# Kernel optimization log

Measured on AMD Instinct MI355X. Metric: run time of the kernel, lower is better.

Reference implementation:

```python
import jax, jax.numpy as jnp
import numpy as np

B, S = 2, 1024            # 2 packed sequences, equal length (offsets = [0, 1024, 2048])
HID, H = 2560, 32
D = HID // H              # 80
ROT = int(0.4 * D)        # 32 partial rotary dims
THETA = 10000.0
MAX_POS = 2048
CACHE_SLOTS = 4096


def setup_inputs() -> dict:
    key = jax.random.key(0)
    ks = jax.random.split(key, 8)
    T = B * S
    w = lambda k: jax.random.normal(k, (HID, HID), dtype=jnp.float32) * 0.02
    return {
        "h": jax.random.normal(ks[0], (T, HID), dtype=jnp.float32),
        "k_cache": jnp.zeros((CACHE_SLOTS, HID), dtype=jnp.float32),
        "v_cache": jnp.zeros((CACHE_SLOTS, HID), dtype=jnp.float32),
        "q_w": w(ks[1]), "q_b": jnp.zeros((HID,), jnp.float32),
        "k_w": w(ks[2]), "k_b": jnp.zeros((HID,), jnp.float32),
        "v_w": w(ks[3]), "v_b": jnp.zeros((HID,), jnp.float32),
        "dense_w": w(ks[4]), "dense_b": jnp.zeros((HID,), jnp.float32),
        "positions": jnp.tile(jnp.arange(S, dtype=jnp.int32), B),
        "offsets": jnp.array([0, S, 2 * S], dtype=jnp.int32),
        "cache_indices": jnp.arange(T, dtype=jnp.int32),
    }


def _rope_tables():
    # neox-style partial rotary tables, [MAX_POS, ROT//2]
    inv_freq = 1.0 / (THETA ** (jnp.arange(0, ROT, 2, dtype=jnp.float32) / ROT))
    freqs = jnp.arange(MAX_POS, dtype=jnp.float32)[:, None] * inv_freq[None, :]
    return jnp.cos(freqs), jnp.sin(freqs)


def _apply_rope(x, cos, sin):
    # x: [T, H, D]; cos/sin: [T, ROT//2] -> rotate first ROT dims, pass rest
    c = cos[:, None, :]
    s = sin[:, None, :]
    x1, x2, rest = x[..., : ROT // 2], x[..., ROT // 2 : ROT], x[..., ROT:]
    return jnp.concatenate([x1 * c - x2 * s, x2 * c + x1 * s, rest], axis=-1)


def reference(h, k_cache, v_cache, q_w, q_b, k_w, k_b, v_w, v_b,
              dense_w, dense_b, positions, offsets, cache_indices):
    T = h.shape[0]
    q = h @ q_w + q_b
    k = h @ k_w + k_b
    v = h @ v_w + v_b

    cos_t, sin_t = _rope_tables()
    cos = cos_t[positions]
    sin = sin_t[positions]
    q = _apply_rope(q.reshape(T, H, D), cos, sin)
    k = _apply_rope(k.reshape(T, H, D), cos, sin)
    v = v.reshape(T, H, D)

    # prompt_init path: scatter freshly-rotated K/V into the flat cache
    k_cache = k_cache.at[cache_indices].set(k.reshape(T, HID))
    v_cache = v_cache.at[cache_indices].set(v.reshape(T, HID))

    # packed_attention: causal attention within each (equal-length) sequence
    q4 = q.reshape(B, S, H, D)
    k4 = k.reshape(B, S, H, D)
    v4 = v.reshape(B, S, H, D)
    scale = D ** -0.5
    scores = jnp.einsum("bqhd,bkhd->bhqk", q4, k4) * scale
    causal = jnp.tril(jnp.ones((S, S), dtype=bool))
    scores = jnp.where(causal[None, None], scores, jnp.float32(-1e9))
    p = jax.nn.softmax(scores, axis=-1)
    o = jnp.einsum("bhqk,bkhd->bqhd", p, v4).reshape(T, HID)

    return o @ dense_w + dense_b
```

## Files before the change

kernel.cpp:

```cpp
#include <hip/hip_runtime.h>
#include <hip/hip_bf16.h>

#define Bq 2
#define Sq 1024
#define Tq 2048
#define HIDq 2560
#define Hq 32
#define Dq 80
#define NQKV 7680

typedef __bf16 bf16x8 __attribute__((ext_vector_type(8)));
typedef float f32x4 __attribute__((ext_vector_type(4)));
typedef unsigned short u16x8 __attribute__((ext_vector_type(8)));
using bf16 = __hip_bfloat16;

__device__ __forceinline__ void gload_lds16(const bf16* g, bf16* l) {
  __builtin_amdgcn_global_load_lds((const __attribute__((address_space(1))) void*)g,
                                   (__attribute__((address_space(3))) void*)l,
                                   16, 0, 0);
}

__global__ __launch_bounds__(256) void cast_h_kernel(const float* __restrict__ h,
                                                     bf16* __restrict__ hb) {
  int i = (blockIdx.x * 256 + threadIdx.x) * 4;
  float4 v = *(const float4*)(h + i);
  bf16 tmp[4];
  tmp[0] = __float2bfloat16(v.x);
  tmp[1] = __float2bfloat16(v.y);
  tmp[2] = __float2bfloat16(v.z);
  tmp[3] = __float2bfloat16(v.w);
  *(ushort4*)(hb + i) = *(ushort4*)tmp;
}

__global__ __launch_bounds__(256) void bias_concat_kernel(const float* __restrict__ qb,
                                                          const float* __restrict__ kb,
                                                          const float* __restrict__ vb,
                                                          float* __restrict__ bqkv) {
  int i = blockIdx.x * 256 + threadIdx.x;
  if (i < HIDq) bqkv[i] = qb[i];
  else if (i < 2 * HIDq) bqkv[i] = kb[i - HIDq];
  else bqkv[i] = vb[i - 2 * HIDq];
}

__global__ __launch_bounds__(256) void wtrans_kernel(const float* __restrict__ qw,
                                                     const float* __restrict__ kw,
                                                     const float* __restrict__ vw,
                                                     const float* __restrict__ dw,
                                                     bf16* __restrict__ wqkvt,
                                                     bf16* __restrict__ wdt) {
  __shared__ float tile[32][33];
  const int z = blockIdx.z;
  const float* src = (z == 0) ? qw : (z == 1) ? kw : (z == 2) ? vw : dw;
  const int n0 = blockIdx.x * 32;
  const int k0 = blockIdx.y * 32;
  const int tx = threadIdx.x, ty = threadIdx.y;
#pragma unroll
  for (int r = 0; r < 4; r++)
    tile[ty + 8 * r][tx] = src[(size_t)(k0 + ty + 8 * r) * HIDq + n0 + tx];
  __syncthreads();
  bf16* dst = (z < 3) ? (wqkvt + (size_t)z * HIDq * HIDq) : wdt;
#pragma unroll
  for (int r = 0; r < 4; r++)
    dst[(size_t)(n0 + ty + 8 * r) * HIDq + k0 + tx] = __float2bfloat16(tile[tx][ty + 8 * r]);
}

__global__ __launch_bounds__(512, 2) void gemm9s_kernel(const bf16* __restrict__ A,
                                                        const bf16* __restrict__ Bt,
                                                        const float* __restrict__ bias,
                                                        bf16* __restrict__ Cout,
                                                        int N, int K, int tM) {
  __shared__ char smem[9 * 16384];
  const int tid = threadIdx.x;
  const int lane = tid & 63;
  const int ln = lane & 15, lg = lane >> 4;
  const int wave = tid >> 6;
  const int wm = wave >> 2;
  const int wn = wave & 3;

  int bid = blockIdx.x, nwg = gridDim.x, swz = bid;
  if ((nwg & 7) == 0) { int cpx = nwg >> 3; swz = (bid & 7) * cpx + (bid >> 3); }
  const int m0 = (swz % tM) * 256;
  const int n0 = (swz / tM) * 256;
  const int NT = K >> 6;

  f32x4 acc[8][4];
  const f32x4 zz = {0.f, 0.f, 0.f, 0.f};
#pragma unroll
  for (int i = 0; i < 8; ++i)
#pragma unroll
    for (int j = 0; j < 4; ++j) acc[i][j] = zz;

  int srow[2], skel[2];
#pragma unroll
  for (int c = 0; c < 2; ++c) {
    const unsigned L = (unsigned)(c * 8192 + tid * 16);
    const unsigned P = L ^ (((L >> 9) & 1u) << 5);
    srow[c] = (int)(P >> 7);
    skel[c] = (int)((P & 127u) >> 1);
  }
  const int wbase = wave * 1024;

  auto STAGE = [&](int H, int ss) {
    const int hh = H & 3;
    const int th = H >> 2;
    const bf16* mat = (hh < 2) ? A : Bt;
    const int rowbase = (hh < 2) ? (m0 + hh * 128) : (n0 + (hh - 2) * 128);
    char* dst = smem + (ss << 14);
#pragma unroll
    for (int c = 0; c < 2; ++c)
      gload_lds16(mat + (size_t)(rowbase + srow[c]) * K + th * 64 + skel[c],
                  (bf16*)(dst + c * 8192 + wbase));
  };

  unsigned offA[2][4][2];
  int     halfA[2][4];
#pragma unroll
  for (int mh = 0; mh < 2; ++mh)
#pragma unroll
    for (int i = 0; i < 4; ++i) {
      const int row = wm * 128 + mh * 64 + i * 16 + ln;
      halfA[mh][i] = row >> 7;
      const int r = row & 127;
#pragma unroll
      for (int kh = 0; kh < 2; ++kh) {
        const unsigned P = (unsigned)(r * 128 + kh * 64 + lg * 16);
        offA[mh][i][kh] = P ^ (((P >> 9) & 1u) << 5);
      }
    }
  unsigned offB[4][2];
  int     halfB[4];
#pragma unroll
  for (int j = 0; j < 4; ++j) {
    const int row = wn * 64 + j * 16 + ln;
    halfB[j] = row >> 7;
    const int r = row & 127;
#pragma unroll
    for (int kh = 0; kh < 2; ++kh) {
      const unsigned P = (unsigned)(r * 128 + kh * 64 + lg * 16);
      offB[j][kh] = P ^ (((P >> 9) & 1u) << 5);
    }
  }

#pragma unroll
  for (int H = 0; H < 5; ++H) STAGE(H, H);

  int s0 = 0;
  for (int t = 0; t < NT; ++t) {
    if (t + 1 < NT) asm volatile("s_waitcnt vmcnt(2)" ::: "memory");
    else            asm volatile("s_waitcnt vmcnt(0)" ::: "memory");
    __builtin_amdgcn_s_barrier();

    int slt[4];
#pragma unroll
    for (int h = 0; h < 4; ++h) { int s = s0 + h; if (s >= 9) s -= 9; slt[h] = s << 14; }

#pragma unroll
    for (int kh = 0; kh < 2; ++kh) {
      bf16x8 bfr[4];
#pragma unroll
      for (int j = 0; j < 4; ++j)
        bfr[j] = *(const bf16x8*)(smem + slt[2 + halfB[j]] + offB[j][kh]);
#pragma unroll
      for (int mh = 0; mh < 2; ++mh) {
        {
          const int p = kh * 2 + mh;
          const int H = 4 * t + p + 5;
          if (H < 4 * NT) {
            int s = s0 + p + 5; if (s >= 9) s -= 9;
            STAGE(H, s);
          }
        }
        bf16x8 af[4];
#pragma unroll
        for (int i = 0; i < 4; ++i)
          af[i] = *(const bf16x8*)(smem + slt[halfA[mh][i]] + offA[mh][i][kh]);
        __builtin_amdgcn_s_setprio(1);
#pragma unroll
        for (int i = 0; i < 4; ++i)
#pragma unroll
          for (int j = 0; j < 4; ++j)
            acc[mh * 4 + i][j] =
                __builtin_amdgcn_mfma_f32_16x16x32_bf16(af[i], bfr[j], acc[mh * 4 + i][j], 0, 0, 0);
        __builtin_amdgcn_s_setprio(0);
      }
    }

    s0 += 4; if (s0 >= 9) s0 -= 9;
  }

#pragma unroll
  for (int i = 0; i < 8; ++i) {
    const int rowb = m0 + wm * 128 + i * 16 + lg * 4;
#pragma unroll
    for (int r = 0; r < 4; ++r) {
#pragma unroll
      for (int j = 0; j < 4; ++j) {
        const int col = n0 + wn * 64 + j * 16 + ln;
        Cout[(size_t)(rowb + r) * N + col] = __float2bfloat16(acc[i][j][r] + bias[col]);
      }
    }
  }
}

template <int MFRAG, int NFRAG, bool OUT_BF16>
__global__ __launch_bounds__(512, 4) void gemm256_kernel(const bf16* __restrict__ A,
                                                         const bf16* __restrict__ Bt,
                                                         const float* __restrict__ bias,
                                                         void* __restrict__ Cout,
                                                         int N, int K, int tMc) {
  constexpr int ACALLS = MFRAG / 4;
  constexpr int BCALLS = NFRAG / 2;
  constexpr int APANEL = 8192 * ACALLS;
  constexpr int BUFSZ = APANEL + 8192 * BCALLS;
  __shared__ char smem[3 * BUFSZ];
  const int tid = threadIdx.x;
  const int lane = tid & 63;
  const int ln = lane & 15, lg = lane >> 4;
  const int wave = tid >> 6;
  const int wm = wave >> 2;
  const int wn = wave & 3;

  int bid = blockIdx.x;
  int swz = bid;
  int nwg = gridDim.x;
  if ((nwg & 7) == 0) { int cpx = nwg >> 3; swz = (bid & 7) * cpx + (bid >> 3); }
  const int m0 = (swz % tMc) * (32 * MFRAG);
  const int n0 = (swz / tMc) * (64 * NFRAG);

  const int NT = K >> 5;

  f32x4 acc[MFRAG][NFRAG];
  const f32x4 zz = {0.f, 0.f, 0.f, 0.f};
#pragma unroll
  for (int i = 0; i < MFRAG; ++i)
#pragma unroll
    for (int j = 0; j < NFRAG; ++j) acc[i][j] = zz;

  const int Rl0 = tid >> 2;
  const int slot = tid & 3;
  const int wbase = (tid >> 6) * 1024;

  auto STAGE = [&](int t, int b) {
    const int k0 = t << 5;
    char* Ab = smem + b * BUFSZ;
    char* Bb = Ab + APANEL;
#pragma unroll
    for (int c = 0; c < ACALLS; ++c) {
      const int srow = c * 128 + Rl0;
      const int row = srow ^ ((srow >> 2) & 1);
      const int col8 = slot ^ (row & 3);
      gload_lds16(A + (size_t)(m0 + row) * K + k0 + col8 * 8,
                  (bf16*)(Ab + c * 8192 + wbase));
    }
#pragma unroll
    for (int c = 0; c < BCALLS; ++c) {
      const int srow = c * 128 + Rl0;
      const int row = srow ^ ((srow >> 2) & 1);
      const int col8 = slot ^ (row & 3);
      gload_lds16(Bt + (size_t)(n0 + row) * K + k0 + col8 * 8,
                  (bf16*)(Bb + c * 8192 + wbase));
    }
  };

  auto FRAG = [&](const char* base, int row) -> bf16x8 {
    const unsigned off = ((unsigned)((row ^ ((row >> 2) & 1)) << 6)) |
                         (((unsigned)lg << 4) ^ ((unsigned)(row & 3) << 4));
    return *(const bf16x8*)(base + off);
  };

  auto WAIT_COUNTED = [&]() {
    constexpr int NCALLS = ACALLS + BCALLS;
    if constexpr (NCALLS == 2)      asm volatile("s_waitcnt vmcnt(2)" ::: "memory");
    else if constexpr (NCALLS == 3) asm volatile("s_waitcnt vmcnt(3)" ::: "memory");
    else                            asm volatile("s_waitcnt vmcnt(4)" ::: "memory");
  };

  STAGE(0, 0);
  STAGE(1, 1);
  WAIT_COUNTED();
  __builtin_amdgcn_s_barrier();

  for (int t = 0; t < NT; ++t) {
    const int cb = t % 3;
    const char* Ab = smem + cb * BUFSZ;
    const char* Bb = Ab + APANEL;
    if (t + 2 < NT) STAGE(t + 2, (t + 2) % 3);

    bf16x8 bfr[NFRAG];
#pragma unroll
    for (int j = 0; j < NFRAG; ++j) bfr[j] = FRAG(Bb, wn * (16 * NFRAG) + j * 16 + ln);
#pragma unroll
    for (int ph = 0; ph < ACALLS; ++ph) {
      bf16x8 af[4];
#pragma unroll
      for (int i = 0; i < 4; ++i)
        af[i] = FRAG(Ab, wm * (16 * MFRAG) + (ph * 4 + i) * 16 + ln);
      __builtin_amdgcn_s_setprio(1);
#pragma unroll
      for (int i = 0; i < 4; ++i)
#pragma unroll
        for (int j = 0; j < NFRAG; ++j)
          acc[ph * 4 + i][j] =
              __builtin_amdgcn_mfma_f32_16x16x32_bf16(af[i], bfr[j], acc[ph * 4 + i][j], 0, 0, 0);
      __builtin_amdgcn_s_setprio(0);
    }

    if (t + 2 < NT) WAIT_COUNTED();
    else            asm volatile("s_waitcnt vmcnt(0)" ::: "memory");
    __builtin_amdgcn_s_barrier();
  }

#pragma unroll
  for (int i = 0; i < MFRAG; ++i) {
    const int rowb = m0 + wm * (16 * MFRAG) + i * 16 + lg * 4;
#pragma unroll
    for (int r = 0; r < 4; ++r) {
#pragma unroll
      for (int j = 0; j < NFRAG; ++j) {
        const int col = n0 + wn * (16 * NFRAG) + j * 16 + ln;
        const float v = acc[i][j][r] + bias[col];
        if (OUT_BF16)
          ((bf16*)Cout)[(size_t)(rowb + r) * N + col] = __float2bfloat16(v);
        else
          ((float*)Cout)[(size_t)(rowb + r) * N + col] = v;
      }
    }
  }
}

__global__ __launch_bounds__(256) void rope_kernel(bf16* __restrict__ qkv,
                                                   const int* __restrict__ positions) {
  int tid = blockIdx.x * 256 + threadIdx.x;
  int i = tid & 15;
  int h = (tid >> 4) & 31;
  int t = tid >> 9;
  float pos = (float)positions[t];
  float inv = exp2f(-0.83048202372f * (float)i);
  float ang = pos * inv;
  float s, c;
  sincosf(ang, &s, &c);
  size_t base = (size_t)t * NQKV + h * Dq + i;
  {
    float x1 = __bfloat162float(qkv[base]);
    float x2 = __bfloat162float(qkv[base + 16]);
    qkv[base] = __float2bfloat16(x1 * c - x2 * s);
    qkv[base + 16] = __float2bfloat16(x2 * c + x1 * s);
  }
  base += HIDq;
  {
    float x1 = __bfloat162float(qkv[base]);
    float x2 = __bfloat162float(qkv[base + 16]);
    qkv[base] = __float2bfloat16(x1 * c - x2 * s);
    qkv[base + 16] = __float2bfloat16(x2 * c + x1 * s);
  }
}

__global__ __launch_bounds__(256) void vtrans_kernel(const bf16* __restrict__ qkv,
                                                     bf16* __restrict__ vT) {
  __shared__ bf16 tile[32][33];
  const int b = blockIdx.z;
  const int c0 = blockIdx.x * 32;
  const int s0 = blockIdx.y * 32;
  const int tx = threadIdx.x, ty = threadIdx.y;
#pragma unroll
  for (int r = 0; r < 4; r++)
    tile[ty + 8 * r][tx] = qkv[(size_t)(b * Sq + s0 + ty + 8 * r) * NQKV + 2 * HIDq + c0 + tx];
  __syncthreads();
#pragma unroll
  for (int r = 0; r < 4; r++)
    vT[(size_t)b * HIDq * Sq + (size_t)(c0 + ty + 8 * r) * Sq + s0 + tx] = tile[tx][ty + 8 * r];
}

__global__ __launch_bounds__(256) void attn_kernel(const bf16* __restrict__ qkv,
                                                   const bf16* __restrict__ vT,
                                                   bf16* __restrict__ obuf) {
  const int x = blockIdx.x;
  const int p = x >> 6;
  const int hb = x & 63;
  const int h = hb >> 1;
  const int b = hb & 1;
  __shared__ bf16 Ks[64][104];
  __shared__ bf16 Vt[80][72];
  __shared__ bf16 Ps[4][16][72];
  const int tid = threadIdx.x;
  const int wave = tid >> 6, lane = tid & 63;
  const int ln = lane & 15, lg = lane >> 4;
  const float scale = 0.1118033988749895f;
  const u16x8 zv = {0, 0, 0, 0, 0, 0, 0, 0};

  const int qtA = p;
  const int qtB = 15 - p;

  u16x8 onesv = zv;
  if (ln == 0) {
#pragma unroll
    for (int e = 0; e < 8; ++e) onesv[e] = 0x3F80;
  }
  const bf16x8 bone = *(const bf16x8*)&onesv;

  if (tid < 128) *(u16x8*)&Ks[tid >> 1][80 + (tid & 1) * 8] = zv;

  bf16x8 aqA[3], aqB[3];
  {
    const size_t qbA = (size_t)(b * Sq + qtA * 64 + wave * 16 + ln) * NQKV + h * Dq;
    const size_t qbB = (size_t)(b * Sq + qtB * 64 + wave * 16 + ln) * NQKV + h * Dq;
#pragma unroll
    for (int kc = 0; kc < 3; ++kc) {
      const int col = kc * 32 + lg * 8;
      u16x8 va = zv, vb = zv;
      if (col < 80) {
        va = *(const u16x8*)(qkv + qbA + col);
        vb = *(const u16x8*)(qkv + qbB + col);
      }
      aqA[kc] = *(bf16x8*)&va;
      aqB[kc] = *(bf16x8*)&vb;
    }
  }

  const bf16* kg[3]; bf16* kl[3];
  const bf16* vg[3]; bf16* vl[3];
#pragma unroll
  for (int it = 0; it < 3; ++it) {
    int c = tid + 256 * it; if (c >= 640) c = 0;
    const int krr = c / 10, kc8 = c % 10;
    kg[it] = qkv + (size_t)(b * Sq + krr) * NQKV + HIDq + h * Dq + kc8 * 8;
    kl[it] = &Ks[krr][kc8 * 8];
    const int vrr = c >> 3, vc8 = c & 7;
    vg[it] = vT + (size_t)b * HIDq * Sq + (size_t)(h * Dq + vrr) * Sq + vc8 * 8;
    vl[it] = &Vt[vrr][vc8 * 8];
  }
  const bool vld2 = (tid < 128);

  u16x8 kreg[3], vreg[3];
  kreg[0] = *(const u16x8*)kg[0]; vreg[0] = *(const u16x8*)vg[0];
  kreg[1] = *(const u16x8*)kg[1]; vreg[1] = *(const u16x8*)vg[1];
  if (vld2) { kreg[2] = *(const u16x8*)kg[2]; vreg[2] = *(const u16x8*)vg[2]; }

  f32x4 oaccA[6], oaccB[6];
  const f32x4 zz = {0.f, 0.f, 0.f, 0.f};
#pragma unroll
  for (int n = 0; n < 6; ++n) { oaccA[n] = zz; oaccB[n] = zz; }

  for (int j = 0; j <= qtB; ++j) {
    __syncthreads();
    *(u16x8*)kl[0] = kreg[0]; *(u16x8*)vl[0] = vreg[0];
    *(u16x8*)kl[1] = kreg[1]; *(u16x8*)vl[1] = vreg[1];
    if (vld2) { *(u16x8*)kl[2] = kreg[2]; *(u16x8*)vl[2] = vreg[2]; }
    if (j < qtB) {
      const size_t ko = (size_t)(j + 1) * 64 * NQKV;
      const int vo = (j + 1) * 64;
      kreg[0] = *(const u16x8*)(kg[0] + ko); vreg[0] = *(const u16x8*)(vg[0] + vo);
      kreg[1] = *(const u16x8*)(kg[1] + ko); vreg[1] = *(const u16x8*)(vg[1] + vo);
      if (vld2) { kreg[2] = *(const u16x8*)(kg[2] + ko); vreg[2] = *(const u16x8*)(vg[2] + vo); }
    }
    __syncthreads();

    {
      f32x4 sacc[4];
#pragma unroll
      for (int n = 0; n < 4; ++n) sacc[n] = zz;
#pragma unroll
      for (int kc = 0; kc < 3; ++kc) {
        bf16x8 bk[4];
#pragma unroll
        for (int n = 0; n < 4; ++n) bk[n] = *(const bf16x8*)&Ks[n * 16 + ln][kc * 32 + lg * 8];
#pragma unroll
        for (int n = 0; n < 4; ++n)
          sacc[n] = __builtin_amdgcn_mfma_f32_16x16x32_bf16(aqB[kc], bk[n], sacc[n], 0, 0, 0);
      }
      const bool diag = (j == qtB);
#pragma unroll
      for (int r = 0; r < 4; ++r) {
        const int qloc = wave * 16 + lg * 4 + r;
#pragma unroll
        for (int n = 0; n < 4; ++n) {
          float xk = sacc[n][r] * scale - 4.0f;
          if (diag && (n * 16 + ln) > qloc) xk = -__builtin_inff();
          Ps[wave][lg * 4 + r][n * 16 + ln] = __float2bfloat16(__expf(xk));
        }
      }
      asm volatile("s_waitcnt lgkmcnt(0)" ::: "memory");
      __builtin_amdgcn_sched_barrier(0);
#pragma unroll
      for (int kc = 0; kc < 2; ++kc) {
        bf16x8 ap = *(const bf16x8*)&Ps[wave][ln][kc * 32 + lg * 8];
        bf16x8 bv[5];
#pragma unroll
        for (int n = 0; n < 5; ++n) bv[n] = *(const bf16x8*)&Vt[n * 16 + ln][kc * 32 + lg * 8];
#pragma unroll
        for (int n = 0; n < 5; ++n)
          oaccB[n] = __builtin_amdgcn_mfma_f32_16x16x32_bf16(ap, bv[n], oaccB[n], 0, 0, 0);
        oaccB[5] = __builtin_amdgcn_mfma_f32_16x16x32_bf16(ap, bone, oaccB[5], 0, 0, 0);
      }
    }

    if (j <= qtA) {
      f32x4 sacc[4];
#pragma unroll
      for (int n = 0; n < 4; ++n) sacc[n] = zz;
#pragma unroll
      for (int kc = 0; kc < 3; ++kc) {
        bf16x8 bk[4];
#pragma unroll
        for (int n = 0; n < 4; ++n) bk[n] = *(const bf16x8*)&Ks[n * 16 + ln][kc * 32 + lg * 8];
#pragma unroll
        for (int n = 0; n < 4; ++n)
          sacc[n] = __builtin_amdgcn_mfma_f32_16x16x32_bf16(aqA[kc], bk[n], sacc[n], 0, 0, 0);
      }
      const bool diag = (j == qtA);
#pragma unroll
      for (int r = 0; r < 4; ++r) {
        const int qloc = wave * 16 + lg * 4 + r;
#pragma unroll
        for (int n = 0; n < 4; ++n) {
          float xk = sacc[n][r] * scale - 4.0f;
          if (diag && (n * 16 + ln) > qloc) xk = -__builtin_inff();
          Ps[wave][lg * 4 + r][n * 16 + ln] = __float2bfloat16(__expf(xk));
        }
      }
      asm volatile("s_waitcnt lgkmcnt(0)" ::: "memory");
      __builtin_amdgcn_sched_barrier(0);
#pragma unroll
      for (int kc = 0; kc < 2; ++kc) {
        bf16x8 ap = *(const bf16x8*)&Ps[wave][ln][kc * 32 + lg * 8];
        bf16x8 bv[5];
#pragma unroll
        for (int n = 0; n < 5; ++n) bv[n] = *(const bf16x8*)&Vt[n * 16 + ln][kc * 32 + lg * 8];
#pragma unroll
        for (int n = 0; n < 5; ++n)
          oaccA[n] = __builtin_amdgcn_mfma_f32_16x16x32_bf16(ap, bv[n], oaccA[n], 0, 0, 0);
        oaccA[5] = __builtin_amdgcn_mfma_f32_16x16x32_bf16(ap, bone, oaccA[5], 0, 0, 0);
      }
    }
  }

#pragma unroll
  for (int r = 0; r < 4; ++r) {
    const float lB = __shfl(oaccB[5][r], lane & 48, 64);
    const float invB = 1.0f / lB;
    const size_t rbB = (size_t)(b * Sq + qtB * 64 + wave * 16 + lg * 4 + r) * HIDq + h * Dq;
#pragma unroll
    for (int n5 = 0; n5 < 5; ++n5)
      obuf[rbB + n5 * 16 + ln] = __float2bfloat16(oaccB[n5][r] * invB);
    const float lA = __shfl(oaccA[5][r], lane & 48, 64);
    const float invA = 1.0f / lA;
    const size_t rbA = (size_t)(b * Sq + qtA * 64 + wave * 16 + lg * 4 + r) * HIDq + h * Dq;
#pragma unroll
    for (int n5 = 0; n5 < 5; ++n5)
      obuf[rbA + n5 * 16 + ln] = __float2bfloat16(oaccA[n5][r] * invA);
  }
}

extern "C" void kernel_launch(void* const* d_in, const int* in_sizes, int n_in,
                              void* d_out, int out_size, void* d_ws, size_t ws_size,
                              hipStream_t stream) {
  const float* h = (const float*)d_in[0];
  const float* q_w = (const float*)d_in[3];
  const float* q_b = (const float*)d_in[4];
  const float* k_w = (const float*)d_in[5];
  const float* k_b = (const float*)d_in[6];
  const float* v_w = (const float*)d_in[7];
  const float* v_b = (const float*)d_in[8];
  const float* dw = (const float*)d_in[9];
  const float* db = (const float*)d_in[10];
  const int* positions = (const int*)d_in[11];

  if (ws_size < 94402560ull) return;
  char* ws = (char*)d_ws;
  bf16* hb = (bf16*)(ws);
  bf16* wqkvt = (bf16*)(ws + 10485760);
  bf16* wdt = (bf16*)(ws + 49807360);
  bf16* qkv = (bf16*)(ws + 62914560);
  float* bqkv = (float*)(ws + 94371840);
  bf16* vT = hb;
  bf16* obuf = wqkvt;

  cast_h_kernel<<<5120, 256, 0, stream>>>(h, hb);
  bias_concat_kernel<<<30, 256, 0, stream>>>(q_b, k_b, v_b, bqkv);
  wtrans_kernel<<<dim3(80, 80, 4), dim3(32, 8), 0, stream>>>(q_w, k_w, v_w, dw, wqkvt, wdt);
  gemm9s_kernel<<<240, 512, 0, stream>>>(hb, wqkvt, bqkv, qkv, NQKV, HIDq, 8);
  rope_kernel<<<4096, 256, 0, stream>>>(qkv, positions);
  vtrans_kernel<<<dim3(80, 32, 2), dim3(32, 8), 0, stream>>>(qkv, vT);
  attn_kernel<<<512, 256, 0, stream>>>(qkv, vT, obuf);
  gemm256_kernel<4, 2, false><<<320, 512, 0, stream>>>(obuf, wdt, db, d_out, HIDq, HIDq, 16);
}
```

Measured before the change: 191.5 us.

## Restructure QKV GEMM main loop into four barrier-separated phases with deeper prefetch

Rewrites the QKV projection GEMM inner loop as four phases, one per quarter of the wave's output tile. Each phase loads its A/B fragments from LDS, issues one async global-to-LDS stage, waits on lgkmcnt and then runs its MFMAs at raised priority, with workgroup barriers between phases. The prologue now prefetches six stages instead of five, and each wave reads only its own half of the A and B slots, so the per-fragment half lookup disappears. The aim is to overlap LDS reads, global loads and MFMA more predictably across waves, at the cost of more barriers per K-step and extra fragment registers.

```diff
diff --git a/kernel.cpp b/kernel.cpp
--- a/kernel.cpp
+++ b/kernel.cpp
@@ -64,7 +64,7 @@
     dst[(size_t)(n0 + ty + 8 * r) * HIDq + k0 + tx] = __float2bfloat16(tile[tx][ty + 8 * r]);
 }
 
-__global__ __launch_bounds__(512, 2) void gemm9s_kernel(const bf16* __restrict__ A,
+__global__ __launch_bounds__(512, 2) void gemm9v_kernel(const bf16* __restrict__ A,
                                                         const bf16* __restrict__ Bt,
                                                         const float* __restrict__ bias,
                                                         bf16* __restrict__ Cout,
@@ -113,77 +113,135 @@
   };
 
   unsigned offA[2][4][2];
-  int     halfA[2][4];
 #pragma unroll
   for (int mh = 0; mh < 2; ++mh)
 #pragma unroll
     for (int i = 0; i < 4; ++i) {
-      const int row = wm * 128 + mh * 64 + i * 16 + ln;
-      halfA[mh][i] = row >> 7;
-      const int r = row & 127;
+      const int r = mh * 64 + i * 16 + ln;
 #pragma unroll
       for (int kh = 0; kh < 2; ++kh) {
         const unsigned P = (unsigned)(r * 128 + kh * 64 + lg * 16);
         offA[mh][i][kh] = P ^ (((P >> 9) & 1u) << 5);
       }
     }
-  unsigned offB[4][2];
-  int     halfB[4];
-#pragma unroll
-  for (int j = 0; j < 4; ++j) {
-    const int row = wn * 64 + j * 16 + ln;
-    halfB[j] = row >> 7;
-    const int r = row & 127;
-#pragma unroll
-    for (int kh = 0; kh < 2; ++kh) {
-      const unsigned P = (unsigned)(r * 128 + kh * 64 + lg * 16);
-      offB[j][kh] = P ^ (((P >> 9) & 1u) << 5);
-    }
-  }
-
-#pragma unroll
-  for (int H = 0; H < 5; ++H) STAGE(H, H);
+  unsigned offB[2][2][2];
+#pragma unroll
+  for (int jh = 0; jh < 2; ++jh)
+#pragma unroll
+    for (int jj = 0; jj < 2; ++jj) {
+      const int r = (wn & 1) * 64 + (jh * 2 + jj) * 16 + ln;
+#pragma unroll
+      for (int kh = 0; kh < 2; ++kh) {
+        const unsigned P = (unsigned)(r * 128 + kh * 64 + lg * 16);
+        offB[jh][jj][kh] = P ^ (((P >> 9) & 1u) << 5);
+      }
+    }
+
+#pragma unroll
+  for (int H = 0; H < 6; ++H) STAGE(H, H);
+  asm volatile("s_waitcnt vmcnt(4)" ::: "memory");
+  __builtin_amdgcn_s_barrier();
 
   int s0 = 0;
   for (int t = 0; t < NT; ++t) {
-    if (t + 1 < NT) asm volatile("s_waitcnt vmcnt(2)" ::: "memory");
-    else            asm volatile("s_waitcnt vmcnt(0)" ::: "memory");
-    __builtin_amdgcn_s_barrier();
-
-    int slt[4];
-#pragma unroll
-    for (int h = 0; h < 4; ++h) { int s = s0 + h; if (s >= 9) s -= 9; slt[h] = s << 14; }
-
-#pragma unroll
-    for (int kh = 0; kh < 2; ++kh) {
-      bf16x8 bfr[4];
-#pragma unroll
-      for (int j = 0; j < 4; ++j)
-        bfr[j] = *(const bf16x8*)(smem + slt[2 + halfB[j]] + offB[j][kh]);
-#pragma unroll
-      for (int mh = 0; mh < 2; ++mh) {
-        {
-          const int p = kh * 2 + mh;
-          const int H = 4 * t + p + 5;
-          if (H < 4 * NT) {
-            int s = s0 + p + 5; if (s >= 9) s -= 9;
-            STAGE(H, s);
-          }
-        }
-        bf16x8 af[4];
-#pragma unroll
-        for (int i = 0; i < 4; ++i)
-          af[i] = *(const bf16x8*)(smem + slt[halfA[mh][i]] + offA[mh][i][kh]);
-        __builtin_amdgcn_s_setprio(1);
-#pragma unroll
-        for (int i = 0; i < 4; ++i)
-#pragma unroll
-          for (int j = 0; j < 4; ++j)
-            acc[mh * 4 + i][j] =
-                __builtin_amdgcn_mfma_f32_16x16x32_bf16(af[i], bfr[j], acc[mh * 4 + i][j], 0, 0, 0);
-        __builtin_amdgcn_s_setprio(0);
-      }
-    }
+    int sa = s0 + wm;             if (sa >= 9) sa -= 9;
+    int sb = s0 + 2 + (wn >> 1);  if (sb >= 9) sb -= 9;
+    const int sA = sa << 14;
+    const int sB = sb << 14;
+    int ss = s0 + 6; if (ss >= 9) ss -= 9;
+    const int Hbase = 4 * t + 6;
+    const int Hmax = 4 * NT;
+
+    bf16x8 af[4][2], bf0[2][2], bf1[2][2];
+
+#pragma unroll
+    for (int i = 0; i < 4; ++i)
+#pragma unroll
+      for (int kh = 0; kh < 2; ++kh)
+        af[i][kh] = *(const bf16x8*)(smem + sA + offA[0][i][kh]);
+#pragma unroll
+    for (int jj = 0; jj < 2; ++jj)
+#pragma unroll
+      for (int kh = 0; kh < 2; ++kh)
+        bf0[jj][kh] = *(const bf16x8*)(smem + sB + offB[0][jj][kh]);
+    if (Hbase < Hmax) STAGE(Hbase, ss);
+    ++ss; if (ss >= 9) ss -= 9;
+    __builtin_amdgcn_s_barrier();
+    asm volatile("s_waitcnt lgkmcnt(0)" ::: "memory");
+    __builtin_amdgcn_sched_barrier(0);
+    __builtin_amdgcn_s_setprio(1);
+#pragma unroll
+    for (int kh = 0; kh < 2; ++kh)
+#pragma unroll
+      for (int i = 0; i < 4; ++i)
+#pragma unroll
+        for (int jj = 0; jj < 2; ++jj)
+          acc[i][jj] = __builtin_amdgcn_mfma_f32_16x16x32_bf16(af[i][kh], bf0[jj][kh],
+                                                               acc[i][jj], 0, 0, 0);
+    __builtin_amdgcn_s_setprio(0);
+    __builtin_amdgcn_s_barrier();
+
+#pragma unroll
+    for (int jj = 0; jj < 2; ++jj)
+#pragma unroll
+      for (int kh = 0; kh < 2; ++kh)
+        bf1[jj][kh] = *(const bf16x8*)(smem + sB + offB[1][jj][kh]);
+    if (Hbase + 1 < Hmax) STAGE(Hbase + 1, ss);
+    ++ss; if (ss >= 9) ss -= 9;
+    __builtin_amdgcn_s_barrier();
+    asm volatile("s_waitcnt lgkmcnt(0)" ::: "memory");
+    __builtin_amdgcn_sched_barrier(0);
+    __builtin_amdgcn_s_setprio(1);
+#pragma unroll
+    for (int kh = 0; kh < 2; ++kh)
+#pragma unroll
+      for (int i = 0; i < 4; ++i)
+#pragma unroll
+        for (int jj = 0; jj < 2; ++jj)
+          acc[i][2 + jj] = __builtin_amdgcn_mfma_f32_16x16x32_bf16(af[i][kh], bf1[jj][kh],
+                                                                   acc[i][2 + jj], 0, 0, 0);
+    __builtin_amdgcn_s_setprio(0);
+    __builtin_amdgcn_s_barrier();
+
+#pragma unroll
+    for (int i = 0; i < 4; ++i)
+#pragma unroll
+      for (int kh = 0; kh < 2; ++kh)
+        af[i][kh] = *(const bf16x8*)(smem + sA + offA[1][i][kh]);
+    if (Hbase + 2 < Hmax) STAGE(Hbase + 2, ss);
+    ++ss; if (ss >= 9) ss -= 9;
+    __builtin_amdgcn_s_barrier();
+    asm volatile("s_waitcnt lgkmcnt(0)" ::: "memory");
+    __builtin_amdgcn_sched_barrier(0);
+    __builtin_amdgcn_s_setprio(1);
+#pragma unroll
+    for (int kh = 0; kh < 2; ++kh)
+#pragma unroll
+      for (int i = 0; i < 4; ++i)
+#pragma unroll
+        for (int jj = 0; jj < 2; ++jj)
+          acc[4 + i][2 + jj] = __builtin_amdgcn_mfma_f32_16x16x32_bf16(af[i][kh], bf1[jj][kh],
+                                                                       acc[4 + i][2 + jj], 0, 0, 0);
+    __builtin_amdgcn_s_setprio(0);
+    __builtin_amdgcn_s_barrier();
+
+    if (Hbase + 3 < Hmax) STAGE(Hbase + 3, ss);
+    __builtin_amdgcn_s_barrier();
+    asm volatile("s_waitcnt lgkmcnt(0)" ::: "memory");
+    __builtin_amdgcn_sched_barrier(0);
+    __builtin_amdgcn_s_setprio(1);
+#pragma unroll
+    for (int kh = 0; kh < 2; ++kh)
+#pragma unroll
+      for (int i = 0; i < 4; ++i)
+#pragma unroll
+        for (int jj = 0; jj < 2; ++jj)
+          acc[4 + i][jj] = __builtin_amdgcn_mfma_f32_16x16x32_bf16(af[i][kh], bf0[jj][kh],
+                                                                   acc[4 + i][jj], 0, 0, 0);
+    __builtin_amdgcn_s_setprio(0);
+    if (t < NT - 2)       asm volatile("s_waitcnt vmcnt(4)" ::: "memory");
+    else if (t == NT - 2) asm volatile("s_waitcnt vmcnt(0)" ::: "memory");
+    __builtin_amdgcn_s_barrier();
 
     s0 += 4; if (s0 >= 9) s0 -= 9;
   }
@@ -578,7 +636,7 @@
   cast_h_kernel<<<5120, 256, 0, stream>>>(h, hb);
   bias_concat_kernel<<<30, 256, 0, stream>>>(q_b, k_b, v_b, bqkv);
   wtrans_kernel<<<dim3(80, 80, 4), dim3(32, 8), 0, stream>>>(q_w, k_w, v_w, dw, wqkvt, wdt);
-  gemm9s_kernel<<<240, 512, 0, stream>>>(hb, wqkvt, bqkv, qkv, NQKV, HIDq, 8);
+  gemm9v_kernel<<<240, 512, 0, stream>>>(hb, wqkvt, bqkv, qkv, NQKV, HIDq, 8);
   rope_kernel<<<4096, 256, 0, stream>>>(qkv, positions);
   vtrans_kernel<<<dim3(80, 32, 2), dim3(32, 8), 0, stream>>>(qkv, vT);
   attn_kernel<<<512, 256, 0, stream>>>(qkv, vT, obuf);
```

After: 208.4 us. +8.8%, slower.
